# Kernel optimization log

Hardware: AMD Instinct MI355X
Metric: run time of the kernel (lower is better)

Reference implementation:

```python
import math
import jax, jax.numpy as jnp
import numpy as np

D = 512; H = 8; DH = 64          # d_model, heads, head dim
AB = 8                            # attention block size (BigBird block)
NG, NW, NR = 2, 5, 3              # global / window / random blocks
K = NG + NW + NR                  # attended blocks per query block
NL = 5                            # layers per (encoder|decoder) stack
MAXSEQ = 1024; BS = 4; NM = 4; LAT = 16; FF = 2048


def setup_inputs() -> dict:
    key = jax.random.key(0)
    ks = jax.random.split(key, 20)
    B = 32
    S_enc = MAXSEQ + 1
    nb_enc = (S_enc + AB - 1) // AB   # 129
    nb_dec = MAXSEQ // AB             # 128
    def n(i, shape, s=0.02):
        return jax.random.normal(ks[i], shape, jnp.float32) * s
    return {
        'x': jax.random.normal(ks[0], (B, MAXSEQ, BS * NM), jnp.float32),
        'eps': jax.random.normal(ks[1], (B, LAT), jnp.float32),
        'emb_in': n(2, (S_enc, D)),
        'emb_out': n(3, (MAXSEQ, D)),
        'W_data': n(4, (BS * NM, D)), 'b_data': jnp.zeros((D,), jnp.float32),
        'Wqkv': n(5, (2 * NL, D, 3 * D)), 'bqkv': jnp.zeros((2 * NL, 3 * D), jnp.float32),
        'Wo': n(6, (2 * NL, D, D)), 'bo': jnp.zeros((2 * NL, D), jnp.float32),
        'ln1_g': jnp.ones((2 * NL, D), jnp.float32), 'ln1_b': jnp.zeros((2 * NL, D), jnp.float32),
        'W1': n(7, (2 * NL, D, FF)), 'b1': jnp.zeros((2 * NL, FF), jnp.float32),
        'W2': n(8, (2 * NL, FF, D)), 'b2': jnp.zeros((2 * NL, D), jnp.float32),
        'ln2_g': jnp.ones((2 * NL, D), jnp.float32), 'ln2_b': jnp.zeros((2 * NL, D), jnp.float32),
        'W_mean': n(9, (D, LAT)), 'b_mean': jnp.zeros((LAT,), jnp.float32),
        'W_lv': n(10, (D, LAT)), 'b_lv': jnp.zeros((LAT,), jnp.float32),
        'W_exp': n(11, (LAT, 2 * MAXSEQ)), 'b_exp': jnp.zeros((2 * MAXSEQ,), jnp.float32),
        'W_conv': n(12, (2, D)), 'b_conv': jnp.zeros((D,), jnp.float32),
        'W_seq': n(13, (D, BS * NM)), 'b_seq': jnp.zeros((BS * NM,), jnp.float32),
        'rand_enc': jax.random.randint(ks[14], (nb_enc, NR), 0, nb_enc, jnp.int32),
        'rand_dec': jax.random.randint(ks[15], (nb_dec, NR), 0, nb_dec, jnp.int32),
    }


def _ln(x, g, b):
    m = jnp.mean(x, -1, keepdims=True)
    v = jnp.var(x, -1, keepdims=True)
    return (x - m) * jax.lax.rsqrt(v + 1e-5) * g + b


def _block_index(nb, rand):
    # per query block: NG global blocks, NW window blocks, NR random blocks
    i = jnp.arange(nb)
    g = jnp.broadcast_to(jnp.arange(NG)[None, :], (nb, NG))
    w = i[:, None] + (jnp.arange(NW) - NW // 2)[None, :]
    w_valid = (w >= 0) & (w < nb)
    idx = jnp.concatenate([g, jnp.clip(w, 0, nb - 1), rand], axis=1)          # [nb, K]
    valid = jnp.concatenate([jnp.ones((nb, NG), bool), w_valid,
                             jnp.ones((nb, NR), bool)], axis=1)               # [nb, K]
    return idx, valid


def _sparse_attn(x, Wqkv, bqkv, Wo, bo, rand):
    # BigBird-style block-sparse self attention (global + window + random blocks)
    B, S, _ = x.shape
    nb = (S + AB - 1) // AB
    Sp = nb * AB
    qkv = jnp.pad(x @ Wqkv + bqkv, ((0, 0), (0, Sp - S), (0, 0)))
    q, k, v = jnp.split(qkv, 3, axis=-1)
    def blk(t):  # [B,Sp,D] -> [B,H,nb,AB,DH]
        return t.reshape(B, nb, AB, H, DH).transpose(0, 3, 1, 2, 4)
    q, k, v = blk(q), blk(k), blk(v)
    idx, bvalid = _block_index(nb, rand)
    kg = k[:, :, idx]                      # [B,H,nb,K,AB,DH]
    vg = v[:, :, idx]
    scores = jnp.einsum('bhnqd,bhnkpd->bhnqkp', q, kg) / math.sqrt(DH)  # [B,H,nb,AB,K,AB]
    tok_valid = (jnp.arange(Sp) < S).reshape(nb, AB)
    kmask = bvalid[:, :, None] & tok_valid[idx]                          # [nb,K,AB]
    scores = jnp.where(kmask[None, None, :, None], scores, -1e9)
    attn = jax.nn.softmax(scores.reshape(B, H, nb, AB, K * AB), axis=-1)
    out = jnp.einsum('bhnqk,bhnkd->bhnqd', attn, vg.reshape(B, H, nb, K * AB, DH))
    out = out.transpose(0, 2, 3, 1, 4).reshape(B, Sp, D)[:, :S]
    return out @ Wo + bo


def _layer(x, i, p, rand):
    (Wqkv, bqkv, Wo, bo, ln1_g, ln1_b, W1, b1, W2, b2, ln2_g, ln2_b) = p
    a = _sparse_attn(x, Wqkv[i], bqkv[i], Wo[i], bo[i], rand)
    x = _ln(x + a, ln1_g[i], ln1_b[i])
    f = jax.nn.relu(x @ W1[i] + b1[i]) @ W2[i] + b2[i]
    return _ln(x + f, ln2_g[i], ln2_b[i])


def _forward(x, eps, emb_in, emb_out, W_data, b_data, Wqkv, bqkv, Wo, bo,
             ln1_g, ln1_b, W1, b1, W2, b2, ln2_g, ln2_b, W_mean, b_mean,
             W_lv, b_lv, W_exp, b_exp, W_conv, b_conv, W_seq, b_seq,
             rand_enc, rand_dec):
    B = x.shape[0]
    p = (Wqkv, bqkv, Wo, bo, ln1_g, ln1_b, W1, b1, W2, b2, ln2_g, ln2_b)
    # ---- encode ----
    h = x @ W_data + b_data                                   # [B,1024,512]
    cls = jnp.zeros((B, 1, D), x.dtype)
    h = jnp.concatenate([cls, h], axis=1) + emb_in            # [B,1025,512]
    for i in range(NL):
        h = _layer(h, i, p, rand_enc)
    pooled = h[:, 0]
    mean = pooled @ W_mean + b_mean
    logvar = pooled @ W_lv + b_lv
    # ---- sample (diag-Gaussian rsample) ----
    z = mean + eps * jnp.exp(0.5 * logvar)
    # ---- decode ----
    seq = (z @ W_exp + b_exp).reshape(B, 2, MAXSEQ)           # [B,2,1024]
    d = jnp.einsum('bcs,cd->bsd', seq, W_conv) + b_conv       # 1x1 conv, -> [B,1024,512]
    d = d + emb_out
    for i in range(NL, 2 * NL):
        d = _layer(d, i, p, rand_dec)
    out = d @ W_seq + b_seq                                   # [B,1024,16] (1x1 conv)
    decoded = out.reshape(B, -1, NM)                          # [B,4096,4]
    elbo = jnp.mean(-0.5 * jnp.sum(1.0 + logvar - mean ** 2 - jnp.exp(logvar), axis=1))
    return decoded, elbo


def reference(x, eps, emb_in, emb_out, W_data, b_data, Wqkv, bqkv, Wo, bo,
              ln1_g, ln1_b, W1, b1, W2, b2, ln2_g, ln2_b, W_mean, b_mean,
              W_lv, b_lv, W_exp, b_exp, W_conv, b_conv, W_seq, b_seq,
              rand_enc, rand_dec):
    return _forward(x, eps, emb_in, emb_out, W_data, b_data, Wqkv, bqkv, Wo, bo,
                    ln1_g, ln1_b, W1, b1, W2, b2, ln2_g, ln2_b, W_mean, b_mean,
                    W_lv, b_lv, W_exp, b_exp, W_conv, b_conv, W_seq, b_seq,
                    rand_enc, rand_dec)
```

## Files before the change

kernel.cpp:

```cpp
#include <hip/hip_runtime.h>

typedef unsigned short u16;
typedef __attribute__((ext_vector_type(8))) short short8;
typedef __attribute__((ext_vector_type(4))) float f32x4;

__device__ __forceinline__ float b2f(u16 h) {
  union { unsigned int u; float f; } v; v.u = ((unsigned int)h) << 16; return v.f;
}
__device__ __forceinline__ u16 f2b(float f) {
  union { float f; unsigned int u; } v; v.f = f;
  return (u16)((v.u + 0x7fffu + ((v.u >> 16) & 1u)) >> 16);
}

__device__ __forceinline__ void gload16(const u16* g, u16* l) {
  __builtin_amdgcn_global_load_lds(
      (const __attribute__((address_space(1))) void*)g,
      (__attribute__((address_space(3))) void*)l, 16, 0, 0);
}

#define SENC 1025
#define SPENC 1032
#define NBE 129
#define SDEC 1024
#define NBD 128
#define BATCH 32
#define MENC (BATCH * SPENC)
#define MDEC (BATCH * SDEC)

__global__ void beacon_k(float* out) { if (threadIdx.x == 0) out[0] = 1000.0f; }

__global__ __launch_bounds__(256) void tr_k(const float* __restrict__ W, u16* __restrict__ WT, int K, int N)
{
  __shared__ float sm[32][33];
  int k0 = blockIdx.x * 32, n0 = blockIdx.y * 32;
  const float* Wz = W + (size_t)blockIdx.z * K * N;
  u16* WTz = WT + (size_t)blockIdx.z * K * N;
  int r = threadIdx.x >> 3, c0 = (threadIdx.x & 7) * 4;
  float4 v = *(const float4*)&Wz[(size_t)(k0 + r) * N + n0 + c0];
  sm[r][c0] = v.x; sm[r][c0 + 1] = v.y; sm[r][c0 + 2] = v.z; sm[r][c0 + 3] = v.w;
  __syncthreads();
  ushort4 u;
  u.x = f2b(sm[c0][r]); u.y = f2b(sm[c0 + 1][r]); u.z = f2b(sm[c0 + 2][r]); u.w = f2b(sm[c0 + 3][r]);
  *(ushort4*)&WTz[(size_t)(n0 + r) * K + k0 + c0] = u;
}

__global__ __launch_bounds__(256) void embed_k(const float* __restrict__ x, const float* __restrict__ Wd,
    const float* __restrict__ bd, const float* __restrict__ emb, float* __restrict__ h, u16* __restrict__ hb)
{
  size_t gid = (size_t)blockIdx.x * 256 + threadIdx.x;
  int dd = (int)(gid & 511);
  size_t rs = gid >> 9;
  int s = (int)(rs % SPENC);
  int b = (int)(rs / SPENC);
  float v;
  if (s == 0) {
    v = emb[dd];
  } else if (s < SENC) {
    float acc = bd[dd];
    const float* xr = x + ((size_t)b * 1024 + (s - 1)) * 16;
    #pragma unroll
    for (int j = 0; j < 16; ++j) acc += xr[j] * Wd[j * 512 + dd];
    v = acc + emb[(size_t)s * 512 + dd];
  } else {
    v = 0.f;
  }
  h[gid] = v;
  hb[gid] = f2b(v);
}

template<typename TC, bool RELU, bool RESID, bool ATOMIC>
__global__ __launch_bounds__(512) void mgemm_k(const u16* __restrict__ A, const u16* __restrict__ WT,
    const float* __restrict__ bias, const float* __restrict__ R, TC* __restrict__ C,
    int M, int N, int Kc, int lda, int ldb)
{
  __shared__ __align__(16) u16 sA[3][128 * 32];
  __shared__ __align__(16) u16 sB[3][256 * 32];
  int t = threadIdx.x;

  int gx = gridDim.x;
  int nwg = gx * gridDim.y;
  int flat = blockIdx.y * gx + blockIdx.x;
  int q = nwg >> 3, rr = nwg & 7;
  int xcd = flat & 7, idx = flat >> 3;
  int swz = (xcd < rr ? xcd * (q + 1) : rr * (q + 1) + (xcd - rr) * q) + idx;
  int bx = swz % gx, by = swz / gx;

  int n0 = bx * 256, m0 = by * 128;
  int koff = blockIdx.z * Kc;
  int lane = t & 63, wave = t >> 6;
  int wm = (wave >> 2) * 64, wn = (wave & 3) * 64;
  int quad = lane >> 4, l15 = lane & 15;

  int rA = t >> 2, sc = t & 3;
  int cA = sc ^ ((rA >> 1) & 3);
  int raA = m0 + rA; raA = raA < M ? raA : M - 1;
  const u16* gA  = A  + (size_t)raA * lda + koff + cA * 8;
  const u16* gB0 = WT + (size_t)(n0 + rA) * ldb + koff + cA * 8;
  const u16* gB1 = WT + (size_t)(n0 + 128 + rA) * ldb + koff + cA * 8;

  f32x4 acc[4][4];
  #pragma unroll
  for (int i = 0; i < 4; ++i)
    #pragma unroll
    for (int j = 0; j < 4; ++j) acc[i][j] = (f32x4){0.f, 0.f, 0.f, 0.f};

  const int nt = Kc >> 5;
  gload16(gA,      &sA[0][t * 8]);
  gload16(gB0,     &sB[0][t * 8]);
  gload16(gB1,     &sB[0][(512 + t) * 8]);
  gload16(gA + 32, &sA[1][t * 8]);
  gload16(gB0 + 32,&sB[1][t * 8]);
  gload16(gB1 + 32,&sB[1][(512 + t) * 8]);

  int cur = 0;
  for (int tt = 0; tt < nt; ++tt) {
    if (tt < nt - 1) {
      asm volatile("s_waitcnt vmcnt(3)" ::: "memory");
    } else {
      asm volatile("s_waitcnt vmcnt(0)" ::: "memory");
    }
    __builtin_amdgcn_s_barrier();
    asm volatile("" ::: "memory");
    if (tt + 2 < nt) {
      int k0 = (tt + 2) << 5;
      int nb = tt + 2; nb -= (nb / 3) * 3;
      gload16(gA + k0,  &sA[nb][t * 8]);
      gload16(gB0 + k0, &sB[nb][t * 8]);
      gload16(gB1 + k0, &sB[nb][(512 + t) * 8]);
    }
    short8 af[4], bf[4];
    #pragma unroll
    for (int i = 0; i < 4; ++i) {
      int ra = wm + i * 16 + l15;
      af[i] = *(const short8*)&sA[cur][ra * 32 + (quad ^ ((ra >> 1) & 3)) * 8];
    }
    #pragma unroll
    for (int j = 0; j < 4; ++j) {
      int rb = wn + j * 16 + l15;
      bf[j] = *(const short8*)&sB[cur][rb * 32 + (quad ^ ((rb >> 1) & 3)) * 8];
    }
    __builtin_amdgcn_s_setprio(1);
    #pragma unroll
    for (int i = 0; i < 4; ++i)
      #pragma unroll
      for (int j = 0; j < 4; ++j)
        acc[i][j] = __builtin_amdgcn_mfma_f32_16x16x32_bf16(af[i], bf[j], acc[i][j], 0, 0, 0);
    __builtin_amdgcn_s_setprio(0);
    cur = (cur == 2) ? 0 : cur + 1;
  }

  #pragma unroll
  for (int i = 0; i < 4; ++i) {
    int mBase = m0 + wm + i * 16 + quad * 4;
    #pragma unroll
    for (int r = 0; r < 4; ++r) {
      int m = mBase + r;
      if (m < M) {
        #pragma unroll
        for (int j = 0; j < 4; ++j) {
          int n = n0 + wn + j * 16 + l15;
          if constexpr (ATOMIC) {
            float v = acc[i][j][r];
            if (blockIdx.z == 0) v += bias[n];
            unsafeAtomicAdd(&((float*)C)[(size_t)m * N + n], v);
          } else {
            float v = acc[i][j][r] + bias[n];
            if (RESID) v += R[(size_t)m * N + n];
            if (RELU) v = fmaxf(v, 0.f);
            if constexpr (sizeof(TC) == 2) ((u16*)C)[(size_t)m * N + n] = f2b(v);
            else ((float*)C)[(size_t)m * N + n] = v;
          }
        }
      }
    }
  }
}

__global__ __launch_bounds__(256) void ln_k(float* h, u16* __restrict__ hb,
    const float* __restrict__ g, const float* __restrict__ bb)
{
  __shared__ float rs[256], rq[256];
  float* p = h + (size_t)blockIdx.x * 512;
  u16* pb = hb + (size_t)blockIdx.x * 512;
  int t = threadIdx.x;
  float v0 = p[t], v1 = p[t + 256];
  rs[t] = v0 + v1; rq[t] = v0 * v0 + v1 * v1;
  __syncthreads();
  for (int o = 128; o > 0; o >>= 1) {
    if (t < o) { rs[t] += rs[t + o]; rq[t] += rq[t + o]; }
    __syncthreads();
  }
  float mean = rs[0] * (1.f / 512.f);
  float var = fmaxf(rq[0] * (1.f / 512.f) - mean * mean, 0.f);
  float rinv = rsqrtf(var + 1e-5f);
  float o0 = (v0 - mean) * rinv * g[t] + bb[t];
  float o1 = (v1 - mean) * rinv * g[t + 256] + bb[t + 256];
  p[t] = o0; p[t + 256] = o1;
  pb[t] = f2b(o0); pb[t + 256] = f2b(o1);
}

__global__ __launch_bounds__(64) void attnm_k(const u16* __restrict__ qkv, u16* __restrict__ av,
    const int* __restrict__ rnd, int S, int Sp, int nb)
{
  __shared__ __align__(16) u16 Vt[64 * 104];
  __shared__ __align__(16) u16 Pl[16 * 104];
  __shared__ int sJB[10], sVD[10];
  int t = threadIdx.x;
  int n = blockIdx.x % nb;
  int r1 = blockIdx.x / nb;
  int hh = r1 & 7, b = r1 >> 3;
  const u16* base = qkv + (size_t)b * Sp * 1536;
  int l15 = t & 15, quad = t >> 4;

  if (t < 10) {
    int jb, vd;
    if (t < 2) { jb = t; vd = 1; }
    else if (t < 7) {
      int w = n + t - 4;
      vd = (w >= 0 && w < nb) ? 1 : 0;
      jb = w < 0 ? 0 : (w > nb - 1 ? nb - 1 : w);
    } else { jb = rnd[n * 3 + t - 7]; vd = 1; }
    sJB[t] = jb; sVD[t] = vd;
  }
  {
    f32x4 zz = {0.f, 0.f, 0.f, 0.f};
    *(f32x4*)&Vt[t * 104 + 80] = zz;
    *(f32x4*)&Vt[t * 104 + 88] = zz;
    if (t < 16) {
      *(f32x4*)&Pl[t * 104 + 80] = zz;
      *(f32x4*)&Pl[t * 104 + 88] = zz;
    }
  }
  __syncthreads();

  short8 aq0, aq1;
  {
    const u16* qp = base + (size_t)(n * 8 + (l15 & 7)) * 1536 + hh * 64 + quad * 8;
    aq0 = *(const short8*)qp;
    aq1 = *(const short8*)(qp + 32);
  }

  f32x4 s[5];
  float okm[5];
  #pragma unroll
  for (int tile = 0; tile < 5; ++tile) {
    int kb = tile * 2 + (l15 >> 3);
    int tok = sJB[kb] * 8 + (l15 & 7);
    okm[tile] = (sVD[kb] && tok < S) ? 0.f : -3.0e38f;
    const u16* kp = base + (size_t)tok * 1536 + 512 + hh * 64 + quad * 8;
    short8 k0 = *(const short8*)kp;
    short8 k1 = *(const short8*)(kp + 32);
    f32x4 c = {0.f, 0.f, 0.f, 0.f};
    c = __builtin_amdgcn_mfma_f32_16x16x32_bf16(aq0, k0, c, 0, 0, 0);
    c = __builtin_amdgcn_mfma_f32_16x16x32_bf16(aq1, k1, c, 0, 0, 0);
    s[tile] = c;
  }

  u16 vreg[80];
  #pragma unroll
  for (int vt = 0; vt < 10; ++vt) {
    const u16* vp = base + (size_t)(sJB[vt] * 8) * 1536 + 1024 + hh * 64 + t;
    #pragma unroll
    for (int j = 0; j < 8; ++j) vreg[vt * 8 + j] = vp[(size_t)j * 1536];
  }

  f32x4 mx = {-3.0e38f, -3.0e38f, -3.0e38f, -3.0e38f};
  #pragma unroll
  for (int tile = 0; tile < 5; ++tile) {
    #pragma unroll
    for (int r = 0; r < 4; ++r) {
      float v = s[tile][r] * 0.125f + okm[tile];
      s[tile][r] = v;
      mx[r] = fmaxf(mx[r], v);
    }
  }
  #pragma unroll
  for (int off = 1; off < 16; off <<= 1) {
    #pragma unroll
    for (int r = 0; r < 4; ++r) mx[r] = fmaxf(mx[r], __shfl_xor(mx[r], off));
  }
  f32x4 sm = {0.f, 0.f, 0.f, 0.f};
  #pragma unroll
  for (int tile = 0; tile < 5; ++tile) {
    #pragma unroll
    for (int r = 0; r < 4; ++r) {
      float e = __expf(s[tile][r] - mx[r]);
      s[tile][r] = e;
      sm[r] += e;
    }
  }
  #pragma unroll
  for (int off = 1; off < 16; off <<= 1) {
    #pragma unroll
    for (int r = 0; r < 4; ++r) sm[r] += __shfl_xor(sm[r], off);
  }

  #pragma unroll
  for (int tile = 0; tile < 5; ++tile)
    #pragma unroll
    for (int r = 0; r < 4; ++r)
      Pl[(quad * 4 + r) * 104 + tile * 16 + l15] = f2b(s[tile][r]);

  #pragma unroll
  for (int vt = 0; vt < 10; ++vt) {
    short8 w;
    #pragma unroll
    for (int j = 0; j < 8; ++j) ((u16*)&w)[j] = (short)vreg[vt * 8 + j];
    *(short8*)&Vt[t * 104 + vt * 8] = w;
  }
  __syncthreads();

  f32x4 o[4];
  #pragma unroll
  for (int dn = 0; dn < 4; ++dn) o[dn] = (f32x4){0.f, 0.f, 0.f, 0.f};
  #pragma unroll
  for (int ks = 0; ks < 3; ++ks) {
    short8 ap = *(const short8*)&Pl[l15 * 104 + ks * 32 + quad * 8];
    #pragma unroll
    for (int dn = 0; dn < 4; ++dn) {
      short8 bv = *(const short8*)&Vt[(dn * 16 + l15) * 104 + ks * 32 + quad * 8];
      o[dn] = __builtin_amdgcn_mfma_f32_16x16x32_bf16(ap, bv, o[dn], 0, 0, 0);
    }
  }

  if (quad < 2) {
    #pragma unroll
    for (int r = 0; r < 4; ++r) {
      int qi = quad * 4 + r;
      float inv = 1.f / sm[r];
      u16* op = av + ((size_t)b * Sp + n * 8 + qi) * 512 + hh * 64 + l15;
      #pragma unroll
      for (int dn = 0; dn < 4; ++dn)
        op[dn * 16] = f2b(o[dn][r] * inv);
    }
  }
}

__global__ __launch_bounds__(512) void head_k(const float* __restrict__ h,
    const float* __restrict__ Wm, const float* __restrict__ bm,
    const float* __restrict__ Wlv, const float* __restrict__ blv,
    const float* __restrict__ eps, float* __restrict__ z, float* out_elbo)
{
  __shared__ float red[512];
  int t = threadIdx.x;
  int b = t >> 4, i = t & 15;
  const float* p = h + (size_t)b * SPENC * 512;
  float am = bm[i], al = blv[i];
  for (int c = 0; c < 512; ++c) {
    float pv = p[c];
    am += pv * Wm[c * 16 + i];
    al += pv * Wlv[c * 16 + i];
  }
  z[t] = am + eps[t] * expf(0.5f * al);
  red[t] = -0.5f * (1.f + al - am * am - expf(al));
  __syncthreads();
  for (int o = 256; o > 0; o >>= 1) { if (t < o) red[t] += red[t + o]; __syncthreads(); }
  if (t == 0) out_elbo[0] = red[0] * (1.f / 32.f);
}

__global__ __launch_bounds__(256) void seq_k(const float* __restrict__ z, const float* __restrict__ We,
    const float* __restrict__ be, float* __restrict__ seq)
{
  int gid = blockIdx.x * 256 + threadIdx.x;
  int b = gid >> 11, c = gid & 2047;
  float acc = be[c];
  #pragma unroll
  for (int i = 0; i < 16; ++i) acc += z[b * 16 + i] * We[i * 2048 + c];
  seq[gid] = acc;
}

__global__ __launch_bounds__(256) void decinit_k(const float* __restrict__ seq, const float* __restrict__ Wc,
    const float* __restrict__ bc, const float* __restrict__ emb, float* __restrict__ h, u16* __restrict__ hb)
{
  size_t gid = (size_t)blockIdx.x * 256 + threadIdx.x;
  int dd = (int)(gid & 511);
  size_t rs = gid >> 9;
  int s = (int)(rs & 1023);
  int b = (int)(rs >> 10);
  float v = seq[b * 2048 + s] * Wc[dd] + seq[b * 2048 + 1024 + s] * Wc[512 + dd]
          + bc[dd] + emb[(size_t)s * 512 + dd];
  h[gid] = v;
  hb[gid] = f2b(v);
}

__global__ __launch_bounds__(256) void final_k(const float* __restrict__ h, const float* __restrict__ Ws,
    const float* __restrict__ bs, float* __restrict__ out)
{
  int gid = blockIdx.x * 256 + threadIdx.x;
  int nn = gid & 15;
  int rs = gid >> 4;
  const float* p = h + (size_t)rs * 512;
  float acc = bs[nn];
  for (int c = 0; c < 512; ++c) acc += p[c] * Ws[c * 16 + nn];
  out[gid] = acc;
}

extern "C" void kernel_launch(void* const* d_in, const int* in_sizes, int n_in,
                              void* d_out, int out_size, void* d_ws, size_t ws_size,
                              hipStream_t stream) {
  float* out = (float*)d_out;
  (void)out_size; (void)ws_size;

  static const int EXP_DICT[30] = {
    524288, 512, 524800, 524288, 8192, 512, 7864320, 15360, 2621440, 5120,
    5120, 5120, 10485760, 20480, 10485760, 5120, 5120, 5120, 8192, 16,
    8192, 16, 32768, 2048, 1024, 512, 8192, 16, 387, 384 };
  bool dict_ok = (n_in == 30);
  if (dict_ok) for (int i = 0; i < 30; ++i) if (in_sizes[i] != EXP_DICT[i]) { dict_ok = false; break; }
  if (!dict_ok) { beacon_k<<<1, 64, 0, stream>>>(out); return; }

  const float* x      = (const float*)d_in[0];
  const float* eps    = (const float*)d_in[1];
  const float* emb_in = (const float*)d_in[2];
  const float* emb_out= (const float*)d_in[3];
  const float* W_data = (const float*)d_in[4];
  const float* b_data = (const float*)d_in[5];
  const float* Wqkv   = (const float*)d_in[6];
  const float* bqkv   = (const float*)d_in[7];
  const float* Wo     = (const float*)d_in[8];
  const float* bo     = (const float*)d_in[9];
  const float* ln1g   = (const float*)d_in[10];
  const float* ln1b   = (const float*)d_in[11];
  const float* W1     = (const float*)d_in[12];
  const float* b1     = (const float*)d_in[13];
  const float* W2     = (const float*)d_in[14];
  const float* b2     = (const float*)d_in[15];
  const float* ln2g   = (const float*)d_in[16];
  const float* ln2b   = (const float*)d_in[17];
  const float* Wm     = (const float*)d_in[18];
  const float* bm     = (const float*)d_in[19];
  const float* Wlv    = (const float*)d_in[20];
  const float* blv    = (const float*)d_in[21];
  const float* Wexp   = (const float*)d_in[22];
  const float* bexp   = (const float*)d_in[23];
  const float* Wconv  = (const float*)d_in[24];
  const float* bconv  = (const float*)d_in[25];
  const float* Wseq   = (const float*)d_in[26];
  const float* bseq   = (const float*)d_in[27];
  const int* rand_enc = (const int*)d_in[28];
  const int* rand_dec = (const int*)d_in[29];

  char* ws = (char*)d_ws;
  float* h     = (float*)ws;
  u16*   hb    = (u16*)(ws + 67633152);
  u16*   WTqkv = (u16*)(ws + 101449728);
  u16*   WTo   = (u16*)(ws + 117178368);
  u16*   WT1l  = (u16*)(ws + 122421248);
  u16*   WT2l  = (u16*)(ws + 124518400);
  u16*   qkvb  = (u16*)(ws + 126615552);
  u16*   avb   = (u16*)(ws + 126615552 + 50724864);
  u16*   ffnb  = (u16*)(ws + 126615552);
  float* seqb  = (float*)(ws + 194248704);
  float* z     = (float*)(ws + 194510848);

  tr_k<<<dim3(512 / 32, 1536 / 32, 10), 256, 0, stream>>>(Wqkv, WTqkv, 512, 1536);
  tr_k<<<dim3(512 / 32, 512 / 32, 10), 256, 0, stream>>>(Wo, WTo, 512, 512);

  {
    const int M = MENC;
    embed_k<<<(M * 512) / 256, 256, 0, stream>>>(x, W_data, b_data, emb_in, h, hb);
    for (int i = 0; i < 5; ++i) {
      for (int bc = 0; bc < 2; ++bc) {
        size_t roff = (size_t)bc * 16 * SPENC * 512;
        const int Mc = 16 * SPENC;
        const int ty = 129;
        mgemm_k<u16, false, false, false><<<dim3(1536 / 256, ty, 1), 512, 0, stream>>>(
            hb + roff, WTqkv + (size_t)i * 512 * 1536, bqkv + (size_t)i * 1536, nullptr, qkvb, Mc, 1536, 512, 512, 512);
        attnm_k<<<16 * 8 * NBE, 64, 0, stream>>>(qkvb, avb, rand_enc, SENC, SPENC, NBE);
        mgemm_k<float, false, false, true><<<dim3(512 / 256, ty, 2), 512, 0, stream>>>(
            avb, WTo + (size_t)i * 512 * 512, bo + (size_t)i * 512, nullptr, h + roff, Mc, 512, 256, 512, 512);
      }
      ln_k<<<M, 256, 0, stream>>>(h, hb, ln1g + (size_t)i * 512, ln1b + (size_t)i * 512);
      tr_k<<<dim3(512 / 32, 2048 / 32, 1), 256, 0, stream>>>(W1 + (size_t)i * 512 * 2048, WT1l, 512, 2048);
      tr_k<<<dim3(2048 / 32, 512 / 32, 1), 256, 0, stream>>>(W2 + (size_t)i * 2048 * 512, WT2l, 2048, 512);
      for (int off = 0; off < M; off += 16512) {
        const int Mc = 16512;
        const int ty = 129;
        mgemm_k<u16, true, false, false><<<dim3(2048 / 256, ty, 1), 512, 0, stream>>>(
            hb + (size_t)off * 512, WT1l, b1 + (size_t)i * 2048, nullptr, ffnb, Mc, 2048, 512, 512, 512);
        mgemm_k<float, false, false, true><<<dim3(512 / 256, ty, 2), 512, 0, stream>>>(
            ffnb, WT2l, b2 + (size_t)i * 512, nullptr, h + (size_t)off * 512, Mc, 512, 1024, 2048, 2048);
      }
      ln_k<<<M, 256, 0, stream>>>(h, hb, ln2g + (size_t)i * 512, ln2b + (size_t)i * 512);
    }
  }

  head_k<<<1, 512, 0, stream>>>(h, Wm, bm, Wlv, blv, eps, z, out + 524288);
  seq_k<<<256, 256, 0, stream>>>(z, Wexp, bexp, seqb);
  decinit_k<<<(MDEC * 512) / 256, 256, 0, stream>>>(seqb, Wconv, bconv, emb_out, h, hb);

  {
    const int M = MDEC;
    for (int i = 5; i < 10; ++i) {
      for (int bc = 0; bc < 2; ++bc) {
        size_t roff = (size_t)bc * 16 * SDEC * 512;
        const int Mc = 16 * SDEC;
        const int ty = 128;
        mgemm_k<u16, false, false, false><<<dim3(1536 / 256, ty, 1), 512, 0, stream>>>(
            hb + roff, WTqkv + (size_t)i * 512 * 1536, bqkv + (size_t)i * 1536, nullptr, qkvb, Mc, 1536, 512, 512, 512);
        attnm_k<<<16 * 8 * NBD, 64, 0, stream>>>(qkvb, avb, rand_dec, SDEC, SDEC, NBD);
        mgemm_k<float, false, false, true><<<dim3(512 / 256, ty, 2), 512, 0, stream>>>(
            avb, WTo + (size_t)i * 512 * 512, bo + (size_t)i * 512, nullptr, h + roff, Mc, 512, 256, 512, 512);
      }
      ln_k<<<M, 256, 0, stream>>>(h, hb, ln1g + (size_t)i * 512, ln1b + (size_t)i * 512);
      tr_k<<<dim3(512 / 32, 2048 / 32, 1), 256, 0, stream>>>(W1 + (size_t)i * 512 * 2048, WT1l, 512, 2048);
      tr_k<<<dim3(2048 / 32, 512 / 32, 1), 256, 0, stream>>>(W2 + (size_t)i * 2048 * 512, WT2l, 2048, 512);
      for (int off = 0; off < M; off += 16384) {
        const int Mc = 16384;
        const int ty = 128;
        mgemm_k<u16, true, false, false><<<dim3(2048 / 256, ty, 1), 512, 0, stream>>>(
            hb + (size_t)off * 512, WT1l, b1 + (size_t)i * 2048, nullptr, ffnb, Mc, 2048, 512, 512, 512);
        mgemm_k<float, false, false, true><<<dim3(512 / 256, ty, 2), 512, 0, stream>>>(
            ffnb, WT2l, b2 + (size_t)i * 512, nullptr, h + (size_t)off * 512, Mc, 512, 1024, 2048, 2048);
      }
      ln_k<<<M, 256, 0, stream>>>(h, hb, ln2g + (size_t)i * 512, ln2b + (size_t)i * 512);
    }
  }

  final_k<<<524288 / 256, 256, 0, stream>>>(h, Wseq, bseq, out);
}
```

Before: 6.723 ms.

## Replace split-K atomic residual GEMMs with bf16 outputs fused into residual-add LayerNorm

The Wo and W2 projections no longer use split-K with float atomic adds into the residual stream. They now run the full K in one pass and write bf16 results to a temporary buffer. A new LayerNorm kernel adds that temporary to the fp32 residual, normalises using wave shuffles instead of a shared-memory tree, and runs per chunk right after its GEMM. FFN chunking changes to three chunks so the temp buffer fits in the workspace. This removes atomic traffic and a separate full read-modify-write of h, but the projection output is rounded to bf16 before the residual add and each GEMM gets fewer workgroups.

```diff
diff --git a/kernel.cpp b/kernel.cpp
--- a/kernel.cpp
+++ b/kernel.cpp
@@ -68,9 +68,9 @@
   hb[gid] = f2b(v);
 }
 
-template<typename TC, bool RELU, bool RESID, bool ATOMIC>
+template<bool RELU>
 __global__ __launch_bounds__(512) void mgemm_k(const u16* __restrict__ A, const u16* __restrict__ WT,
-    const float* __restrict__ bias, const float* __restrict__ R, TC* __restrict__ C,
+    const float* __restrict__ bias, u16* __restrict__ C,
     int M, int N, int Kc, int lda, int ldb)
 {
   __shared__ __align__(16) u16 sA[3][128 * 32];
@@ -86,7 +86,6 @@
   int bx = swz % gx, by = swz / gx;
 
   int n0 = bx * 256, m0 = by * 128;
-  int koff = blockIdx.z * Kc;
   int lane = t & 63, wave = t >> 6;
   int wm = (wave >> 2) * 64, wn = (wave & 3) * 64;
   int quad = lane >> 4, l15 = lane & 15;
@@ -94,9 +93,9 @@
   int rA = t >> 2, sc = t & 3;
   int cA = sc ^ ((rA >> 1) & 3);
   int raA = m0 + rA; raA = raA < M ? raA : M - 1;
-  const u16* gA  = A  + (size_t)raA * lda + koff + cA * 8;
-  const u16* gB0 = WT + (size_t)(n0 + rA) * ldb + koff + cA * 8;
-  const u16* gB1 = WT + (size_t)(n0 + 128 + rA) * ldb + koff + cA * 8;
+  const u16* gA  = A  + (size_t)raA * lda + cA * 8;
+  const u16* gB0 = WT + (size_t)(n0 + rA) * ldb + cA * 8;
+  const u16* gB1 = WT + (size_t)(n0 + 128 + rA) * ldb + cA * 8;
 
   f32x4 acc[4][4];
   #pragma unroll
@@ -159,44 +158,45 @@
         #pragma unroll
         for (int j = 0; j < 4; ++j) {
           int n = n0 + wn + j * 16 + l15;
-          if constexpr (ATOMIC) {
-            float v = acc[i][j][r];
-            if (blockIdx.z == 0) v += bias[n];
-            unsafeAtomicAdd(&((float*)C)[(size_t)m * N + n], v);
-          } else {
-            float v = acc[i][j][r] + bias[n];
-            if (RESID) v += R[(size_t)m * N + n];
-            if (RELU) v = fmaxf(v, 0.f);
-            if constexpr (sizeof(TC) == 2) ((u16*)C)[(size_t)m * N + n] = f2b(v);
-            else ((float*)C)[(size_t)m * N + n] = v;
-          }
+          float v = acc[i][j][r] + bias[n];
+          if (RELU) v = fmaxf(v, 0.f);
+          C[(size_t)m * N + n] = f2b(v);
         }
       }
     }
   }
 }
 
-__global__ __launch_bounds__(256) void ln_k(float* h, u16* __restrict__ hb,
-    const float* __restrict__ g, const float* __restrict__ bb)
-{
-  __shared__ float rs[256], rq[256];
+__global__ __launch_bounds__(256) void lnf_k(float* __restrict__ h, const u16* __restrict__ tmp,
+    u16* __restrict__ hb, const float* __restrict__ g, const float* __restrict__ bb)
+{
+  __shared__ float ls[4], lq[4];
+  int t = threadIdx.x;
   float* p = h + (size_t)blockIdx.x * 512;
+  const u16* tp = tmp + (size_t)blockIdx.x * 512;
   u16* pb = hb + (size_t)blockIdx.x * 512;
-  int t = threadIdx.x;
-  float v0 = p[t], v1 = p[t + 256];
-  rs[t] = v0 + v1; rq[t] = v0 * v0 + v1 * v1;
+  float2 hv = *(const float2*)&p[2 * t];
+  ushort2 tv = *(const ushort2*)&tp[2 * t];
+  float v0 = hv.x + b2f(tv.x);
+  float v1 = hv.y + b2f(tv.y);
+  float s = v0 + v1, qq = v0 * v0 + v1 * v1;
+  #pragma unroll
+  for (int off = 1; off < 64; off <<= 1) {
+    s += __shfl_xor(s, off);
+    qq += __shfl_xor(qq, off);
+  }
+  if ((t & 63) == 0) { ls[t >> 6] = s; lq[t >> 6] = qq; }
   __syncthreads();
-  for (int o = 128; o > 0; o >>= 1) {
-    if (t < o) { rs[t] += rs[t + o]; rq[t] += rq[t + o]; }
-    __syncthreads();
-  }
-  float mean = rs[0] * (1.f / 512.f);
-  float var = fmaxf(rq[0] * (1.f / 512.f) - mean * mean, 0.f);
+  s = ls[0] + ls[1] + ls[2] + ls[3];
+  qq = lq[0] + lq[1] + lq[2] + lq[3];
+  float mean = s * (1.f / 512.f);
+  float var = fmaxf(qq * (1.f / 512.f) - mean * mean, 0.f);
   float rinv = rsqrtf(var + 1e-5f);
-  float o0 = (v0 - mean) * rinv * g[t] + bb[t];
-  float o1 = (v1 - mean) * rinv * g[t + 256] + bb[t + 256];
-  p[t] = o0; p[t + 256] = o1;
-  pb[t] = f2b(o0); pb[t + 256] = f2b(o1);
+  float o0 = (v0 - mean) * rinv * g[2 * t] + bb[2 * t];
+  float o1 = (v1 - mean) * rinv * g[2 * t + 1] + bb[2 * t + 1];
+  *(float2*)&p[2 * t] = make_float2(o0, o1);
+  ushort2 ob; ob.x = f2b(o0); ob.y = f2b(o1);
+  *(ushort2*)&pb[2 * t] = ob;
 }
 
 __global__ __launch_bounds__(64) void attnm_k(const u16* __restrict__ qkv, u16* __restrict__ av,
@@ -449,7 +449,9 @@
   u16*   WT2l  = (u16*)(ws + 124518400);
   u16*   qkvb  = (u16*)(ws + 126615552);
   u16*   avb   = (u16*)(ws + 126615552 + 50724864);
+  u16*   tmpo  = (u16*)(ws + 126615552);
   u16*   ffnb  = (u16*)(ws + 126615552);
+  u16*   tmpF  = (u16*)(ws + 126615552 + 45088768);
   float* seqb  = (float*)(ws + 194248704);
   float* z     = (float*)(ws + 194510848);
 
@@ -464,24 +466,25 @@
         size_t roff = (size_t)bc * 16 * SPENC * 512;
         const int Mc = 16 * SPENC;
         const int ty = 129;
-        mgemm_k<u16, false, false, false><<<dim3(1536 / 256, ty, 1), 512, 0, stream>>>(
-            hb + roff, WTqkv + (size_t)i * 512 * 1536, bqkv + (size_t)i * 1536, nullptr, qkvb, Mc, 1536, 512, 512, 512);
+        mgemm_k<false><<<dim3(6, ty), 512, 0, stream>>>(
+            hb + roff, WTqkv + (size_t)i * 512 * 1536, bqkv + (size_t)i * 1536, qkvb, Mc, 1536, 512, 512, 512);
         attnm_k<<<16 * 8 * NBE, 64, 0, stream>>>(qkvb, avb, rand_enc, SENC, SPENC, NBE);
-        mgemm_k<float, false, false, true><<<dim3(512 / 256, ty, 2), 512, 0, stream>>>(
-            avb, WTo + (size_t)i * 512 * 512, bo + (size_t)i * 512, nullptr, h + roff, Mc, 512, 256, 512, 512);
+        mgemm_k<false><<<dim3(2, ty), 512, 0, stream>>>(
+            avb, WTo + (size_t)i * 512 * 512, bo + (size_t)i * 512, tmpo, Mc, 512, 512, 512, 512);
+        lnf_k<<<Mc, 256, 0, stream>>>(h + roff, tmpo, hb + roff, ln1g + (size_t)i * 512, ln1b + (size_t)i * 512);
       }
-      ln_k<<<M, 256, 0, stream>>>(h, hb, ln1g + (size_t)i * 512, ln1b + (size_t)i * 512);
       tr_k<<<dim3(512 / 32, 2048 / 32, 1), 256, 0, stream>>>(W1 + (size_t)i * 512 * 2048, WT1l, 512, 2048);
       tr_k<<<dim3(2048 / 32, 512 / 32, 1), 256, 0, stream>>>(W2 + (size_t)i * 2048 * 512, WT2l, 2048, 512);
-      for (int off = 0; off < M; off += 16512) {
-        const int Mc = 16512;
-        const int ty = 129;
-        mgemm_k<u16, true, false, false><<<dim3(2048 / 256, ty, 1), 512, 0, stream>>>(
-            hb + (size_t)off * 512, WT1l, b1 + (size_t)i * 2048, nullptr, ffnb, Mc, 2048, 512, 512, 512);
-        mgemm_k<float, false, false, true><<<dim3(512 / 256, ty, 2), 512, 0, stream>>>(
-            ffnb, WT2l, b2 + (size_t)i * 512, nullptr, h + (size_t)off * 512, Mc, 512, 1024, 2048, 2048);
+      for (int cc = 0; cc < 3; ++cc) {
+        size_t off = (size_t)cc * 11008;
+        const int Mc = 11008;
+        const int ty = 86;
+        mgemm_k<true><<<dim3(8, ty), 512, 0, stream>>>(
+            hb + off * 512, WT1l, b1 + (size_t)i * 2048, ffnb, Mc, 2048, 512, 512, 512);
+        mgemm_k<false><<<dim3(2, ty), 512, 0, stream>>>(
+            ffnb, WT2l, b2 + (size_t)i * 512, tmpF, Mc, 512, 2048, 2048, 2048);
+        lnf_k<<<Mc, 256, 0, stream>>>(h + off * 512, tmpF, hb + off * 512, ln2g + (size_t)i * 512, ln2b + (size_t)i * 512);
       }
-      ln_k<<<M, 256, 0, stream>>>(h, hb, ln2g + (size_t)i * 512, ln2b + (size_t)i * 512);
     }
   }
 
@@ -490,30 +493,32 @@
   decinit_k<<<(MDEC * 512) / 256, 256, 0, stream>>>(seqb, Wconv, bconv, emb_out, h, hb);
 
   {
-    const int M = MDEC;
     for (int i = 5; i < 10; ++i) {
       for (int bc = 0; bc < 2; ++bc) {
         size_t roff = (size_t)bc * 16 * SDEC * 512;
         const int Mc = 16 * SDEC;
         const int ty = 128;
-        mgemm_k<u16, false, false, false><<<dim3(1536 / 256, ty, 1), 512, 0, stream>>>(
-            hb + roff, WTqkv + (size_t)i * 512 * 1536, bqkv + (size_t)i * 1536, nullptr, qkvb, Mc, 1536, 512, 512, 512);
+        mgemm_k<false><<<dim3(6, ty), 512, 0, stream>>>(
+            hb + roff, WTqkv + (size_t)i * 512 * 1536, bqkv + (size_t)i * 1536, qkvb, Mc, 1536, 512, 512, 512);
         attnm_k<<<16 * 8 * NBD, 64, 0, stream>>>(qkvb, avb, rand_dec, SDEC, SDEC, NBD);
-        mgemm_k<float, false, false, true><<<dim3(512 / 256, ty, 2), 512, 0, stream>>>(
-            avb, WTo + (size_t)i * 512 * 512, bo + (size_t)i * 512, nullptr, h + roff, Mc, 512, 256, 512, 512);
+        mgemm_k<false><<<dim3(2, ty), 512, 0, stream>>>(
+            avb, WTo + (size_t)i * 512 * 512, bo + (size_t)i * 512, tmpo, Mc, 512, 512, 512, 512);
+        lnf_k<<<Mc, 256, 0, stream>>>(h + roff, tmpo, hb + roff, ln1g + (size_t)i * 512, ln1b + (size_t)i * 512);
       }
-      ln_k<<<M, 256, 0, stream>>>(h, hb, ln1g + (size_t)i * 512, ln1b + (size_t)i * 512);
       tr_k<<<dim3(512 / 32, 2048 / 32, 1), 256, 0, stream>>>(W1 + (size_t)i * 512 * 2048, WT1l, 512, 2048);
       tr_k<<<dim3(2048 / 32, 512 / 32, 1), 256, 0, stream>>>(W2 + (size_t)i * 2048 * 512, WT2l, 2048, 512);
-      for (int off = 0; off < M; off += 16384) {
-        const int Mc = 16384;
-        const int ty = 128;
-        mgemm_k<u16, true, false, false><<<dim3(2048 / 256, ty, 1), 512, 0, stream>>>(
-            hb + (size_t)off * 512, WT1l, b1 + (size_t)i * 2048, nullptr, ffnb, Mc, 2048, 512, 512, 512);
-        mgemm_k<float, false, false, true><<<dim3(512 / 256, ty, 2), 512, 0, stream>>>(
-            ffnb, WT2l, b2 + (size_t)i * 512, nullptr, h + (size_t)off * 512, Mc, 512, 1024, 2048, 2048);
+      static const int DOFF[3] = {0, 11008, 22016};
+      static const int DMC[3]  = {11008, 11008, 10752};
+      for (int cc = 0; cc < 3; ++cc) {
+        size_t off = (size_t)DOFF[cc];
+        const int Mc = DMC[cc];
+        const int ty = Mc / 128;
+        mgemm_k<true><<<dim3(8, ty), 512, 0, stream>>>(
+            hb + off * 512, WT1l, b1 + (size_t)i * 2048, ffnb, Mc, 2048, 512, 512, 512);
+        mgemm_k<false><<<dim3(2, ty), 512, 0, stream>>>(
+            ffnb, WT2l, b2 + (size_t)i * 512, tmpF, Mc, 512, 2048, 2048, 2048);
+        lnf_k<<<Mc, 256, 0, stream>>>(h + off * 512, tmpF, hb + off * 512, ln2g + (size_t)i * 512, ln2b + (size_t)i * 512);
       }
-      ln_k<<<M, 256, 0, stream>>>(h, hb, ln2g + (size_t)i * 512, ln2b + (size_t)i * 512);
     }
   }
 
```

Result: faster. 6.140 ms (-8.7%).
